# Kernel tuning notes

Hardware: AMD Instinct MI355X
Metric: run time of the kernel (lower is better)

## Reference

```python
import jax, jax.numpy as jnp
import numpy as np

N_NODES = 100000
N_EDGES = 1600000
D = 128
BETA = 0.001
EPS = 1e-12  # F.normalize eps


def setup_inputs() -> dict:
    key = jax.random.key(0)
    k1, k2, k3, k4, k5, k6 = jax.random.split(key, 6)
    stdv = 1.0 / np.sqrt(D)
    return {
        "input": jax.random.normal(k1, (N_NODES, D), dtype=jnp.float32),
        "edge_rows": jax.random.randint(k2, (N_EDGES,), 0, N_NODES, dtype=jnp.int32),
        "edge_cols": jax.random.randint(k3, (N_EDGES,), 0, N_NODES, dtype=jnp.int32),
        "edge_vals": jax.random.uniform(k4, (N_EDGES,), dtype=jnp.float32),
        "weight": jax.random.uniform(k5, (D, D), minval=-stdv, maxval=stdv, dtype=jnp.float32),
        "bias": jax.random.uniform(k6, (D,), minval=-stdv, maxval=stdv, dtype=jnp.float32),
    }


def reference(input, edge_rows, edge_cols, edge_vals, weight, bias):
    # dense projection: [N, D]
    support = input @ weight
    # sparse neighbor aggregation: agg[i] = sum_{(i,j) in E} adj_val * support[j]
    msgs = edge_vals[:, None] * support[edge_cols]          # [E, D]
    agg = jax.ops.segment_sum(msgs, edge_rows, num_segments=input.shape[0])
    # beta-weighted residual blend
    out = BETA * input + (1.0 - BETA) * agg
    # row-wise L2 normalize (torch F.normalize, p=2, dim=1)
    norm = jnp.sqrt(jnp.sum(out * out, axis=1, keepdims=True))
    out = out / jnp.maximum(norm, EPS)
    # bias add
    return out + bias
```

## Files before the change

kernel.cpp:

```cpp
#include <hip/hip_runtime.h>

#define N_NODES 100000
#define N_EDGES 1600000
#define D 128
#define NB 1563
#define CAP 1280

typedef short bf16x8 __attribute__((ext_vector_type(8)));
typedef float f32x4 __attribute__((ext_vector_type(4)));

__device__ __forceinline__ unsigned short f2bf(float x){
  union { float f; unsigned u; } v; v.f = x;
  unsigned r = v.u + 0x7fffu + ((v.u >> 16) & 1u);
  return (unsigned short)(r >> 16);
}

__device__ __forceinline__ float bf2f(unsigned short h){
  union { unsigned u; float f; } v; v.u = ((unsigned)h) << 16;
  return v.f;
}

__global__ __launch_bounds__(256) void convert_input(const float4* __restrict__ in4,
                                                     ushort4* __restrict__ outb){
  int i = blockIdx.x*256 + threadIdx.x;
  float4 a = in4[i];
  ushort4 h;
  h.x = f2bf(a.x); h.y = f2bf(a.y); h.z = f2bf(a.z); h.w = f2bf(a.w);
  outb[i] = h;
}

__global__ __launch_bounds__(256) void scatter_direct(const int* __restrict__ rows,
                                                      const int* __restrict__ cols,
                                                      const float* __restrict__ vals,
                                                      int* __restrict__ cursor,
                                                      int2* __restrict__ edges_s){
  int i = blockIdx.x*256 + threadIdx.x;
  int r = rows[i];
  int b = r >> 6;
  int pos = atomicAdd(&cursor[b*16], 1);
  if (pos < CAP)
    edges_s[(size_t)b*CAP + pos] =
        make_int2(cols[i] | ((r & 63) << 17), __float_as_int(vals[i]));
}

__global__ __launch_bounds__(256) void sortB_kernel(int2* __restrict__ edges,
                                                    const int* __restrict__ cursor,
                                                    int* __restrict__ row_start,
                                                    int* __restrict__ counts){
  __shared__ int2 st[CAP];
  __shared__ int hist[64];
  __shared__ int cur[64];
  int t = threadIdx.x;
  int b = blockIdx.x;
  int base = b * CAP;
  int m = cursor[b*16];
  if (m > CAP) m = CAP;
  if (t < 64) hist[t] = 0;
  __syncthreads();
  for (int i = t; i < m; i += 256){
    int2 e = edges[base + i];
    st[i] = e;
    atomicAdd(&hist[((unsigned)e.x) >> 17], 1);
  }
  __syncthreads();
  if (t < 64){
    int c = hist[t];
    int x = c;
    #pragma unroll
    for (int off = 1; off < 64; off <<= 1){
      int y = __shfl_up(x, off);
      if (t >= off) x += y;
    }
    int excl = x - c;
    cur[t] = excl;
    int grow = b*64 + t;
    row_start[grow] = base + excl;
    counts[grow] = c;
  }
  __syncthreads();
  for (int i = t; i < m; i += 256){
    int2 e = st[i];
    int r = ((unsigned)e.x) >> 17;
    int pos = atomicAdd(&cur[r], 1);
    edges[base + pos] = make_int2(e.x & 0x1FFFF, e.y);
  }
}

__global__ void transpose_w(const float* __restrict__ W, unsigned short* __restrict__ WT){
  int idx = blockIdx.x*256 + threadIdx.x;
  int k = idx >> 7, c = idx & 127;
  WT[c*128 + k] = f2bf(W[idx]);
}

__global__ __launch_bounds__(256) void agg_kernel(const ushort4* __restrict__ inb4,
                                                  const int* __restrict__ row_start,
                                                  const int* __restrict__ counts,
                                                  const int2* __restrict__ edges,
                                                  ushort4* __restrict__ aggb){
  int g = threadIdx.x >> 5, l = threadIdx.x & 31;
  int row = blockIdx.x*8 + g;
  int start = row_start[row];
  int n = counts[row];
  int e = start, end = start + n;

  float4 a0 = make_float4(0.f,0.f,0.f,0.f);
  float4 a1 = make_float4(0.f,0.f,0.f,0.f);
  float4 a2 = make_float4(0.f,0.f,0.f,0.f);
  float4 a3 = make_float4(0.f,0.f,0.f,0.f);

  for (; e + 4 <= end; e += 4){
    int2 e0 = edges[e+0];
    int2 e1 = edges[e+1];
    int2 e2 = edges[e+2];
    int2 e3 = edges[e+3];
    ushort4 x0 = inb4[(size_t)e0.x*32 + l];
    ushort4 x1 = inb4[(size_t)e1.x*32 + l];
    ushort4 x2 = inb4[(size_t)e2.x*32 + l];
    ushort4 x3 = inb4[(size_t)e3.x*32 + l];
    float v0 = __int_as_float(e0.y), v1 = __int_as_float(e1.y);
    float v2 = __int_as_float(e2.y), v3 = __int_as_float(e3.y);
    a0.x = fmaf(v0, bf2f(x0.x), a0.x); a0.y = fmaf(v0, bf2f(x0.y), a0.y);
    a0.z = fmaf(v0, bf2f(x0.z), a0.z); a0.w = fmaf(v0, bf2f(x0.w), a0.w);
    a1.x = fmaf(v1, bf2f(x1.x), a1.x); a1.y = fmaf(v1, bf2f(x1.y), a1.y);
    a1.z = fmaf(v1, bf2f(x1.z), a1.z); a1.w = fmaf(v1, bf2f(x1.w), a1.w);
    a2.x = fmaf(v2, bf2f(x2.x), a2.x); a2.y = fmaf(v2, bf2f(x2.y), a2.y);
    a2.z = fmaf(v2, bf2f(x2.z), a2.z); a2.w = fmaf(v2, bf2f(x2.w), a2.w);
    a3.x = fmaf(v3, bf2f(x3.x), a3.x); a3.y = fmaf(v3, bf2f(x3.y), a3.y);
    a3.z = fmaf(v3, bf2f(x3.z), a3.z); a3.w = fmaf(v3, bf2f(x3.w), a3.w);
  }
  for (; e < end; ++e){
    int2 ee = edges[e];
    ushort4 x = inb4[(size_t)ee.x*32 + l];
    float v = __int_as_float(ee.y);
    a0.x = fmaf(v, bf2f(x.x), a0.x); a0.y = fmaf(v, bf2f(x.y), a0.y);
    a0.z = fmaf(v, bf2f(x.z), a0.z); a0.w = fmaf(v, bf2f(x.w), a0.w);
  }
  float4 s;
  s.x = (a0.x + a1.x) + (a2.x + a3.x);
  s.y = (a0.y + a1.y) + (a2.y + a3.y);
  s.z = (a0.z + a1.z) + (a2.z + a3.z);
  s.w = (a0.w + a1.w) + (a2.w + a3.w);
  ushort4 h;
  h.x = f2bf(s.x); h.y = f2bf(s.y); h.z = f2bf(s.z); h.w = f2bf(s.w);
  aggb[(size_t)row*32 + l] = h;
}

__global__ __launch_bounds__(256) void final_kernel(const ushort4* __restrict__ aggb,
                                                    const float* __restrict__ input,
                                                    const unsigned short* __restrict__ WT,
                                                    const float* __restrict__ bias,
                                                    float* __restrict__ out){
  __shared__ unsigned short Ws[128*136];
  __shared__ unsigned short As[64*136];
  int t = threadIdx.x;
  int block_row = blockIdx.x * 64;

  const ushort4* WT4 = (const ushort4*)WT;
  #pragma unroll
  for (int i = 0; i < 16; ++i){
    int idx4 = i*256 + t;
    int c = idx4 >> 5, k4 = idx4 & 31;
    ushort4 w = WT4[idx4];
    *((ushort4*)&Ws[c*136 + k4*4]) = w;
  }
  #pragma unroll
  for (int i = 0; i < 8; ++i){
    int idx4 = i*256 + t;
    int row = idx4 >> 5, k4 = idx4 & 31;
    int grow = block_row + row;
    ushort4 h = make_ushort4(0,0,0,0);
    if (grow < N_NODES) h = aggb[(size_t)grow*32 + k4];
    *((ushort4*)&As[row*136 + k4*4]) = h;
  }
  __syncthreads();

  int wave = t >> 6, lane = t & 63;
  int q = lane >> 4, n = lane & 15;

  bf16x8 afr[4];
  #pragma unroll
  for (int ks = 0; ks < 4; ++ks)
    afr[ks] = *((const bf16x8*)&As[(wave*16 + n)*136 + ks*32 + q*8]);

  f32x4 acc[8];
  #pragma unroll
  for (int ct = 0; ct < 8; ++ct) acc[ct] = (f32x4){0.f, 0.f, 0.f, 0.f};

  #pragma unroll
  for (int ct = 0; ct < 8; ++ct){
    #pragma unroll
    for (int ks = 0; ks < 4; ++ks){
      bf16x8 bfr = *((const bf16x8*)&Ws[(ct*16 + n)*136 + ks*32 + q*8]);
      acc[ct] = __builtin_amdgcn_mfma_f32_16x16x32_bf16(afr[ks], bfr, acc[ct], 0, 0, 0);
    }
  }

  int base_row = block_row + wave*16 + q*4;
  float v[8][4];
  float s[4] = {0.f, 0.f, 0.f, 0.f};
  #pragma unroll
  for (int reg = 0; reg < 4; ++reg){
    int grow = base_row + reg;
    const float* inrow = input + (size_t)grow * D;
    #pragma unroll
    for (int ct = 0; ct < 8; ++ct){
      float inp = (grow < N_NODES) ? inrow[ct*16 + n] : 0.f;
      float val = fmaf(0.999f, acc[ct][reg], 0.001f * inp);
      v[ct][reg] = val;
      s[reg] = fmaf(val, val, s[reg]);
    }
  }
  #pragma unroll
  for (int reg = 0; reg < 4; ++reg){
    float x = s[reg];
    x += __shfl_xor(x, 1);
    x += __shfl_xor(x, 2);
    x += __shfl_xor(x, 4);
    x += __shfl_xor(x, 8);
    s[reg] = x;
  }
  #pragma unroll
  for (int reg = 0; reg < 4; ++reg){
    int grow = base_row + reg;
    if (grow >= N_NODES) continue;
    float scale = 1.f / fmaxf(sqrtf(s[reg]), 1e-12f);
    float* outrow = out + (size_t)grow * D;
    #pragma unroll
    for (int ct = 0; ct < 8; ++ct){
      outrow[ct*16 + n] = fmaf(v[ct][reg], scale, bias[ct*16 + n]);
    }
  }
}

extern "C" void kernel_launch(void* const* d_in, const int* in_sizes, int n_in,
                              void* d_out, int out_size, void* d_ws, size_t ws_size,
                              hipStream_t stream){
  const float* input  = (const float*)d_in[0];
  const int*   erows  = (const int*)d_in[1];
  const int*   ecols  = (const int*)d_in[2];
  const float* evals  = (const float*)d_in[3];
  const float* weight = (const float*)d_in[4];
  const float* bias   = (const float*)d_in[5];
  float* out = (float*)d_out;

  int*   cursor    = (int*)d_ws;
  int*   row_start = cursor + NB*16;
  int*   counts    = row_start + NB*64;
  int2*  edges_s   = (int2*)(counts + NB*64);
  ushort4* aggb    = (ushort4*)(edges_s + (size_t)NB*CAP);
  ushort4* inb     = aggb + (size_t)N_NODES * 32;
  unsigned short* WTg = (unsigned short*)(inb + (size_t)N_NODES * 32);

  hipMemsetAsync(cursor, 0, NB * 16 * sizeof(int), stream);
  convert_input<<<12500, 256, 0, stream>>>((const float4*)input, inb);
  scatter_direct<<<N_EDGES/256, 256, 0, stream>>>(erows, ecols, evals, cursor, edges_s);
  sortB_kernel<<<NB, 256, 0, stream>>>(edges_s, cursor, row_start, counts);
  transpose_w<<<64, 256, 0, stream>>>(weight, WTg);
  agg_kernel<<<N_NODES/8, 256, 0, stream>>>(inb, row_start, counts, edges_s, aggb);
  final_kernel<<<(N_NODES + 63)/64, 256, 0, stream>>>(aggb, input, WTg, bias, out);
}
```

Measured before the change: 351.0 us.

## Split per-bucket scatter cursors into sub-buckets to reduce atomic contention

The scatter kernel now picks one of eight sub-buckets per bucket from the block index, each with its own cursor and fixed sub-capacity. The goal is to spread atomicAdd traffic over more addresses and cut contention on the per-bucket counters. The sort kernel collects the sub-buckets into shared memory before building the histogram. Cursors are now densely packed instead of padded by 16, so counters of neighbouring buckets share cache lines. The fixed sub-capacity of 224 is a risk: a skewed sub-bucket would silently drop edges.

```diff
diff --git a/kernel.cpp b/kernel.cpp
--- a/kernel.cpp
+++ b/kernel.cpp
@@ -4,7 +4,10 @@
 #define N_EDGES 1600000
 #define D 128
 #define NB 1563
-#define CAP 1280
+#define NSUB 8
+#define SUBCAP 224
+#define CAP (NSUB*SUBCAP)
+#define STAGE 1536
 
 typedef short bf16x8 __attribute__((ext_vector_type(8)));
 typedef float f32x4 __attribute__((ext_vector_type(4)));
@@ -35,11 +38,12 @@
                                                       int* __restrict__ cursor,
                                                       int2* __restrict__ edges_s){
   int i = blockIdx.x*256 + threadIdx.x;
+  int s = blockIdx.x & (NSUB-1);
   int r = rows[i];
   int b = r >> 6;
-  int pos = atomicAdd(&cursor[b*16], 1);
-  if (pos < CAP)
-    edges_s[(size_t)b*CAP + pos] =
+  int pos = atomicAdd(&cursor[s*NB + b], 1);
+  if (pos < SUBCAP)
+    edges_s[(size_t)b*CAP + s*SUBCAP + pos] =
         make_int2(cols[i] | ((r & 63) << 17), __float_as_int(vals[i]));
 }
 
@@ -47,29 +51,35 @@
                                                     const int* __restrict__ cursor,
                                                     int* __restrict__ row_start,
                                                     int* __restrict__ counts){
-  __shared__ int2 st[CAP];
+  __shared__ int2 st[STAGE];
   __shared__ int hist[64];
   __shared__ int cur[64];
   int t = threadIdx.x;
   int b = blockIdx.x;
   int base = b * CAP;
-  int m = cursor[b*16];
-  if (m > CAP) m = CAP;
   if (t < 64) hist[t] = 0;
   __syncthreads();
-  for (int i = t; i < m; i += 256){
-    int2 e = edges[base + i];
-    st[i] = e;
-    atomicAdd(&hist[((unsigned)e.x) >> 17], 1);
-  }
+  int off = 0;
+  #pragma unroll
+  for (int s = 0; s < NSUB; ++s){
+    int ms = cursor[s*NB + b];
+    if (ms > SUBCAP) ms = SUBCAP;
+    for (int i = t; i < ms; i += 256){
+      int2 e = edges[base + s*SUBCAP + i];
+      st[off + i] = e;
+      atomicAdd(&hist[((unsigned)e.x) >> 17], 1);
+    }
+    off += ms;
+  }
+  int m = off;
   __syncthreads();
   if (t < 64){
     int c = hist[t];
     int x = c;
     #pragma unroll
-    for (int off = 1; off < 64; off <<= 1){
-      int y = __shfl_up(x, off);
-      if (t >= off) x += y;
+    for (int o = 1; o < 64; o <<= 1){
+      int y = __shfl_up(x, o);
+      if (t >= o) x += y;
     }
     int excl = x - c;
     cur[t] = excl;
@@ -244,14 +254,14 @@
   float* out = (float*)d_out;
 
   int*   cursor    = (int*)d_ws;
-  int*   row_start = cursor + NB*16;
+  int*   row_start = cursor + NSUB*NB;
   int*   counts    = row_start + NB*64;
   int2*  edges_s   = (int2*)(counts + NB*64);
   ushort4* aggb    = (ushort4*)(edges_s + (size_t)NB*CAP);
   ushort4* inb     = aggb + (size_t)N_NODES * 32;
   unsigned short* WTg = (unsigned short*)(inb + (size_t)N_NODES * 32);
 
-  hipMemsetAsync(cursor, 0, NB * 16 * sizeof(int), stream);
+  hipMemsetAsync(cursor, 0, NSUB * NB * sizeof(int), stream);
   convert_input<<<12500, 256, 0, stream>>>((const float4*)input, inb);
   scatter_direct<<<N_EDGES/256, 256, 0, stream>>>(erows, ecols, evals, cursor, edges_s);
   sortB_kernel<<<NB, 256, 0, stream>>>(edges_s, cursor, row_start, counts);
```

After: 328.8 us. -6.3%, faster.
